# Performance work log

Hardware: AMD Instinct MI355X
Metric: run time of the kernel (lower is better)

## Reference

```python
import jax, jax.numpy as jnp
import numpy as np
from jax import lax

BETA = 0.5          # module default beta
WD_ITERATION = 50   # module default wd_iteration
ERR_TOL = 0.1       # early-exit threshold in IPOT loop
EPS_FILL = 1e-8     # masked_fill value


def setup_inputs() -> dict:
    key = jax.random.key(0)
    k1, k2 = jax.random.split(key)
    bs, N = 128, 512
    # non-negative cost matrix, bs x N x N
    C = jax.random.uniform(k1, (bs, N, N), dtype=jnp.float32)
    # boolean node mask, bs x N; guarantee at least one valid node per graph
    mask = jax.random.uniform(k2, (bs, N)) < 0.8
    mask = mask.at[:, 0].set(True)
    return {"C": C, "bs": bs, "N_s": N, "N_t": N, "mask": mask}


def _ipot_T(C, mask, beta=BETA, iteration=WD_ITERATION):
    m = mask.astype(jnp.float32)                                   # (bs, N)
    mu = (m / jnp.sum(m, axis=1, keepdims=True))[:, :, None]       # (bs, N, 1)
    mv = mu
    T0 = m[:, :, None] * m[:, None, :]                             # bmm(mask, mask^T)
    A = jnp.exp(-C / beta)
    notmask = ~mask[:, :, None]                                    # (bs, N, 1)

    def step(carry, _):
        T, sigma, done = carry
        Q = A * T
        b = jnp.einsum('bnm,bmk->bnk', Q, sigma)                   # Q @ sigma
        b = jnp.where(notmask, EPS_FILL, b)
        delta = mu / b
        a = jnp.einsum('bnm,bnk->bmk', Q, delta)                   # Q^T @ delta
        a = jnp.where(notmask, EPS_FILL, a)
        sigma_new = mv / a
        T_new = delta * Q * jnp.swapaxes(sigma_new, 1, 2)
        err = jnp.max(jnp.sum(jnp.abs(T_new - T), axis=-1))        # global max, as in torch
        # emulate host-side early exit: once converged, freeze state
        T_out = jnp.where(done, T, T_new)
        sigma_out = jnp.where(done, sigma, sigma_new)
        done_out = done | (err < ERR_TOL)
        return (T_out, sigma_out, done_out), None

    (T, _, _), _ = lax.scan(step, (T0, mu, jnp.array(False)), None, length=iteration)
    return T


def reference(C, bs, N_s, N_t, mask):
    T = _ipot_T(C, mask)
    distance = jnp.sum(T * C, axis=(-2, -1))                       # (bs,)
    return (distance, T, C)
```

## Files before the change

kernel.cpp:

```cpp
#include <hip/hip_runtime.h>

#define INVB   2.0f
#define TOL    0.1f
#define EPS    1e-8f
#define NITER  50


__device__ __forceinline__ float wave_sum(float v) {
    for (int o = 32; o > 0; o >>= 1) v += __shfl_down(v, o, 64);
    return v;
}

__global__ __launch_bounds__(1024, 4) void k_ipot_blk(
    const float* __restrict__ C, const void* __restrict__ mraw,
    int bs, int N, float* outD, float* outT, float* outC)
{
    const int bb   = blockIdx.x;
    const int t    = threadIdx.x;
    const int lane = t & 63;
    const int wv   = t >> 6;
    const int nw   = blockDim.x >> 6;
    const float NEG = -__builtin_inff();

    __shared__ __align__(16) float m01[512];
    __shared__ __align__(16) float ld_s[512];
    __shared__ __align__(16) float ldp_s[512];
    __shared__ __align__(16) float ls_s[512];
    __shared__ __align__(16) float lsp_s[512];
    __shared__ __align__(16) float lsig_s[512];
    __shared__ __align__(16) float bv_s[512];
    __shared__ __align__(16) float ap_s[1024];
    __shared__ float red_s[16];
    __shared__ unsigned errbits;
    __shared__ int sF_flag, sB_flag;
    __shared__ float muv_s, lmu_s;

    if (t == 0) { sF_flag = 0; sB_flag = 0; }
    __syncthreads();
    {
        const unsigned* mw = (const unsigned*)mraw;
        const int nwords = (bs * N) >> 2;
        int f = 0, b = 0;
        for (int i = t; i < nwords; i += 1024) {
            unsigned w = mw[i];
            if (w == 0x3f800000u) f = 1;
            else if (w > 1u)      b = 1;
        }
        if (f) atomicOr(&sF_flag, 1);
        if (b) atomicOr(&sB_flag, 1);
    }
    __syncthreads();
    const int mode = sF_flag ? 2 : (sB_flag ? 1 : 0);

    if (t < N) {
        const int idx = bb * N + t;
        bool mv;
        if (mode == 1)      mv = ((const unsigned char*)mraw)[idx] != 0;
        else if (mode == 2) mv = ((const float*)mraw)[idx] != 0.0f;
        else                mv = ((const int*)mraw)[idx] != 0;
        const float z = mv ? 0.f : NEG;
        m01[t]  = mv ? 1.f : 0.f;
        ld_s[t] = z;  ldp_s[t] = z;
        ls_s[t] = z;  lsp_s[t] = z;
    }
    __syncthreads();
    if (wv < (N >> 6)) {
        float v = (t < N) ? m01[t] : 0.f;
        v = wave_sum(v);
        if (lane == 0) red_s[wv] = v;
    }
    __syncthreads();
    if (t == 0) {
        float cnt = 0.f;
        for (int i = 0; i < (N >> 6); ++i) cnt += red_s[i];
        const float muv = 1.0f / cnt;
        muv_s = muv; lmu_s = __logf(muv);
    }
    __syncthreads();
    const float muv = muv_s, lmu = lmu_s;
    if (t < N) lsig_s[t] = (m01[t] != 0.f) ? lmu : NEG;
    __syncthreads();

    const int rpw = N / nw;

    for (int j = 0; j < rpw; ++j) {
        const int n = wv * rpw + j;
        float acc = 0.f;
        if (m01[n] != 0.f) {
            const float* crow = C + ((size_t)bb * N + n) * N;
            for (int m = lane * 4; m < N; m += 256) {
                float4 c4 = *(const float4*)(crow + m);
                float4 m4 = *(const float4*)(&m01[m]);
                acc += m4.x * __expf(lmu - INVB * c4.x);
                acc += m4.y * __expf(lmu - INVB * c4.y);
                acc += m4.z * __expf(lmu - INVB * c4.z);
                acc += m4.w * __expf(lmu - INVB * c4.w);
            }
        }
        acc = wave_sum(acc);
        if (lane == 0) bv_s[n] = acc;
    }
    __syncthreads();

    int kf = NITER;
    for (int it = 0; it < NITER; ++it) {
        const float s1 = (float)it * INVB;
        const float s2 = s1 + INVB;
        const float s3 = s2 + INVB;

        if (t < N) {
            const bool v = m01[t] != 0.f;
            const float mun = v ? muv : 0.f;
            const float bm  = v ? bv_s[t] : EPS;
            const float ldo = ld_s[t];
            ldp_s[t] = ldo;
            ld_s[t]  = ldo + __logf(mun / bm);
        }
        __syncthreads();

        {
            const int h  = t / N;
            const int m  = t - h * N;
            const int n0 = h * (N >> 1);
            const float lsv = ls_s[m];
            const float* cp = C + ((size_t)bb * N + n0) * N + m;
            float acc = 0.f;
            #pragma unroll 8
            for (int i = 0; i < (N >> 1); ++i)
                acc += __expf(ld_s[n0 + i] + lsv - s2 * cp[(size_t)i * N]);
            ap_s[t] = acc;
        }
        __syncthreads();

        if (t < N) {
            const bool v = m01[t] != 0.f;
            const float av  = ap_s[t] + ap_s[t + N];
            const float am  = v ? av : EPS;
            const float mun = v ? muv : 0.f;
            const float lsg = __logf(mun / am);
            const float lso = ls_s[t];
            lsp_s[t]  = lso;
            ls_s[t]   = lso + lsg;
            lsig_s[t] = lsg;
        }
        if (t == 0) errbits = 0u;
        __syncthreads();

        {
            float errmax = 0.f;
            for (int j = 0; j < rpw; ++j) {
                const int n = wv * rpw + j;
                const float ldn = ld_s[n], ldo = ldp_s[n];
                float eacc = 0.f, bacc = 0.f;
                if (m01[n] != 0.f) {
                    const float* crow = C + ((size_t)bb * N + n) * N;
                    for (int m = lane * 4; m < N; m += 256) {
                        float4 c4  = *(const float4*)(crow + m);
                        float4 ln4 = *(const float4*)(&ls_s[m]);
                        float4 lo4 = *(const float4*)(&lsp_s[m]);
                        float4 lg4 = *(const float4*)(&lsig_s[m]);
                        float tn, to;
                        tn = __expf(ldn + ln4.x - s2 * c4.x);
                        to = __expf(ldo + lo4.x - s1 * c4.x);
                        eacc += fabsf(tn - to);
                        bacc += __expf(ldn + ln4.x + lg4.x - s3 * c4.x);
                        tn = __expf(ldn + ln4.y - s2 * c4.y);
                        to = __expf(ldo + lo4.y - s1 * c4.y);
                        eacc += fabsf(tn - to);
                        bacc += __expf(ldn + ln4.y + lg4.y - s3 * c4.y);
                        tn = __expf(ldn + ln4.z - s2 * c4.z);
                        to = __expf(ldo + lo4.z - s1 * c4.z);
                        eacc += fabsf(tn - to);
                        bacc += __expf(ldn + ln4.z + lg4.z - s3 * c4.z);
                        tn = __expf(ldn + ln4.w - s2 * c4.w);
                        to = __expf(ldo + lo4.w - s1 * c4.w);
                        eacc += fabsf(tn - to);
                        bacc += __expf(ldn + ln4.w + lg4.w - s3 * c4.w);
                    }
                }
                bacc = wave_sum(bacc);
                eacc = wave_sum(eacc);
                if (lane == 0) { bv_s[n] = bacc; errmax = fmaxf(errmax, eacc); }
            }
            if (lane == 0) atomicMax(&errbits, __float_as_uint(errmax));
        }
        __syncthreads();

        if (__uint_as_float(errbits) < TOL) { kf = it + 1; break; }
    }

    {
        const float sF = (float)kf * INVB;
        for (int j = 0; j < rpw; ++j) {
            const int n  = wv * rpw + j;
            const int gr = bb * N + n;
            const float ldv = ld_s[n];
            const float* crow = C + (size_t)gr * N;
            float* trow = outT + (size_t)gr * N;
            float* orow = outC + (size_t)gr * N;
            float acc = 0.f;
            for (int m = lane * 4; m < N; m += 256) {
                float4 c4 = *(const float4*)(crow + m);
                float4 l4 = *(const float4*)(&ls_s[m]);
                float4 t4;
                t4.x = __expf(ldv + l4.x - sF * c4.x);
                t4.y = __expf(ldv + l4.y - sF * c4.y);
                t4.z = __expf(ldv + l4.z - sF * c4.z);
                t4.w = __expf(ldv + l4.w - sF * c4.w);
                acc += t4.x * c4.x + t4.y * c4.y + t4.z * c4.z + t4.w * c4.w;
                *(float4*)(trow + m) = t4;
                *(float4*)(orow + m) = c4;
            }
            acc = wave_sum(acc);
            if (lane == 0) bv_s[n] = acc;
        }
    }
    __syncthreads();

    if (t < 256 && t + 256 < N) bv_s[t] += bv_s[t + 256];
    __syncthreads();
    for (int o = 128; o > 0; o >>= 1) {
        if (t < o) bv_s[t] += bv_s[t + o];
        __syncthreads();
    }
    if (t == 0) outD[bb] = bv_s[0];
}

extern "C" void kernel_launch(void* const* d_in, const int* in_sizes, int n_in,
                              void* d_out, int out_size, void* d_ws, size_t ws_size,
                              hipStream_t stream) {
    const float* C    = (const float*)d_in[0];
    const void*  mask = d_in[4];
    const int R  = in_sizes[4];
    const int N  = in_sizes[0] / R;
    const int bs = R / N;

    float* outD = (float*)d_out;
    float* outT = outD + bs;
    float* outC = outT + (size_t)bs * N * N;

    k_ipot_blk<<<bs, 1024, 0, stream>>>(C, mask, bs, N, outD, outT, outC);
}
```

Before: 273.9 us.

## Split each batch across four cooperating blocks with global atomic group barriers

Each batch is now handled by four workgroups, each owning a quarter of the rows, instead of one workgroup per batch. This gives 512 blocks rather than 128 so more of the GPU's compute units are used. The column sums that were a separate strided pass are now fused into the row pass, with partial results exchanged through workspace and spin-wait flags. A separate zeroing kernel also detects the mask dtype. The risks are spin-barrier latency on every iteration, a possible deadlock if the four blocks of a group are not co-resident, and the cost of the extra launch.

```diff
diff --git a/kernel.cpp b/kernel.cpp
--- a/kernel.cpp
+++ b/kernel.cpp
@@ -1,229 +1,306 @@
 #include <hip/hip_runtime.h>
 
-#define INVB   2.0f
-#define TOL    0.1f
-#define EPS    1e-8f
-#define NITER  50
-
-
-__device__ __forceinline__ float wave_sum(float v) {
-    for (int o = 32; o > 0; o >>= 1) v += __shfl_down(v, o, 64);
+#define INVB  2.0f
+#define TOL   0.1f
+#define EPS   1e-8f
+#define NITER 50
+#define NP    4
+
+
+__device__ __forceinline__ float wsum(float v) {
+    #pragma unroll
+    for (int o = 1; o < 64; o <<= 1) v += __shfl_xor(v, o, 64);
     return v;
 }
 
-__global__ __launch_bounds__(1024, 4) void k_ipot_blk(
+__device__ __forceinline__ void group_arrive(unsigned* flagp) {
+    __hip_atomic_fetch_add(flagp, 1u, __ATOMIC_RELEASE, __HIP_MEMORY_SCOPE_AGENT);
+}
+__device__ __forceinline__ void group_wait(unsigned* flagp, unsigned target) {
+    long sp = 0;
+    while (__hip_atomic_load(flagp, __ATOMIC_RELAXED, __HIP_MEMORY_SCOPE_AGENT)
+               < target && sp < (1L << 24)) {
+        __builtin_amdgcn_s_sleep(2); ++sp;
+    }
+    (void)__hip_atomic_load(flagp, __ATOMIC_ACQUIRE, __HIP_MEMORY_SCOPE_AGENT);
+}
+
+__global__ void k_zero(unsigned* ctrl, int ctrlwords, int* mode,
+                       const unsigned* mraw, int nwords) {
+    const int t = threadIdx.x;
+    for (int i = t; i < ctrlwords; i += 1024) ctrl[i] = 0u;
+    __shared__ int sF, sB;
+    if (t == 0) { sF = 0; sB = 0; }
+    __syncthreads();
+    int f = 0, b = 0;
+    for (int i = t; i < nwords; i += 1024) {
+        unsigned w = mraw[i];
+        if (w == 0x3f800000u) f = 1;
+        else if (w > 1u)      b = 1;
+    }
+    if (f) atomicOr(&sF, 1);
+    if (b) atomicOr(&sB, 1);
+    __syncthreads();
+    if (t == 0) *mode = sF ? 2 : (sB ? 1 : 0);
+}
+
+__global__ __launch_bounds__(1024, 8) void k_ipot4(
     const float* __restrict__ C, const void* __restrict__ mraw,
-    int bs, int N, float* outD, float* outT, float* outC)
+    int bs, int N,
+    unsigned* err_u, unsigned* flags, float* dpart, const int* mode_p,
+    float* apart, float* outD, float* outT, float* outC)
 {
-    const int bb   = blockIdx.x;
+    const int g    = blockIdx.x >> 2;
+    const int p    = blockIdx.x & 3;
     const int t    = threadIdx.x;
     const int lane = t & 63;
     const int wv   = t >> 6;
-    const int nw   = blockDim.x >> 6;
+    const int NR   = N >> 2;
+    const int r0   = p * NR;
+    const int rpw  = NR >> 4;
     const float NEG = -__builtin_inff();
-
-    __shared__ __align__(16) float m01[512];
-    __shared__ __align__(16) float ld_s[512];
-    __shared__ __align__(16) float ldp_s[512];
+    unsigned* flagp = &flags[g * 16];
+
     __shared__ __align__(16) float ls_s[512];
     __shared__ __align__(16) float lsp_s[512];
     __shared__ __align__(16) float lsig_s[512];
-    __shared__ __align__(16) float bv_s[512];
-    __shared__ __align__(16) float ap_s[1024];
+    __shared__ __align__(16) float m01[512];
+    __shared__ float ld_own[128], ldp_own[128];
+    __shared__ __align__(16) float ap_ws[16][512];
     __shared__ float red_s[16];
-    __shared__ unsigned errbits;
-    __shared__ int sF_flag, sB_flag;
-    __shared__ float muv_s, lmu_s;
-
-    if (t == 0) { sF_flag = 0; sB_flag = 0; }
-    __syncthreads();
+    __shared__ float muv_s, lmu_s, errg_s;
+    __shared__ unsigned errbits_s;
+
     {
-        const unsigned* mw = (const unsigned*)mraw;
-        const int nwords = (bs * N) >> 2;
-        int f = 0, b = 0;
-        for (int i = t; i < nwords; i += 1024) {
-            unsigned w = mw[i];
-            if (w == 0x3f800000u) f = 1;
-            else if (w > 1u)      b = 1;
-        }
-        if (f) atomicOr(&sF_flag, 1);
-        if (b) atomicOr(&sB_flag, 1);
-    }
-    __syncthreads();
-    const int mode = sF_flag ? 2 : (sB_flag ? 1 : 0);
-
-    if (t < N) {
-        const int idx = bb * N + t;
-        bool mv;
-        if (mode == 1)      mv = ((const unsigned char*)mraw)[idx] != 0;
-        else if (mode == 2) mv = ((const float*)mraw)[idx] != 0.0f;
-        else                mv = ((const int*)mraw)[idx] != 0;
-        const float z = mv ? 0.f : NEG;
-        m01[t]  = mv ? 1.f : 0.f;
-        ld_s[t] = z;  ldp_s[t] = z;
-        ls_s[t] = z;  lsp_s[t] = z;
-    }
-    __syncthreads();
-    if (wv < (N >> 6)) {
-        float v = (t < N) ? m01[t] : 0.f;
-        v = wave_sum(v);
-        if (lane == 0) red_s[wv] = v;
-    }
-    __syncthreads();
-    if (t == 0) {
-        float cnt = 0.f;
-        for (int i = 0; i < (N >> 6); ++i) cnt += red_s[i];
-        const float muv = 1.0f / cnt;
-        muv_s = muv; lmu_s = __logf(muv);
-    }
-    __syncthreads();
+        const int mode = *mode_p;
+        if (t < N) {
+            const int idx = g * N + t;
+            bool mv;
+            if (mode == 1)      mv = ((const unsigned char*)mraw)[idx] != 0;
+            else if (mode == 2) mv = ((const float*)mraw)[idx] != 0.0f;
+            else                mv = ((const int*)mraw)[idx] != 0;
+            m01[t] = mv ? 1.f : 0.f;
+            const float z = mv ? 0.f : NEG;
+            ls_s[t] = z; lsp_s[t] = z;
+        }
+        __syncthreads();
+        if (t < N) {
+            float v = wsum(m01[t]);
+            if (lane == 0) red_s[wv] = v;
+        }
+        __syncthreads();
+        if (t == 0) {
+            float cnt = 0.f;
+            for (int i = 0; i < (N >> 6); ++i) cnt += red_s[i];
+            muv_s = 1.0f / cnt;
+            lmu_s = __logf(muv_s);
+        }
+        __syncthreads();
+        if (t < N) lsig_s[t] = (m01[t] != 0.f) ? lmu_s : NEG;
+        if (t < NR) {
+            const float z = (m01[r0 + t] != 0.f) ? 0.f : NEG;
+            ld_own[t] = z; ldp_own[t] = z;
+        }
+        __syncthreads();
+    }
     const float muv = muv_s, lmu = lmu_s;
-    if (t < N) lsig_s[t] = (m01[t] != 0.f) ? lmu : NEG;
-    __syncthreads();
-
-    const int rpw = N / nw;
-
-    for (int j = 0; j < rpw; ++j) {
-        const int n = wv * rpw + j;
-        float acc = 0.f;
-        if (m01[n] != 0.f) {
-            const float* crow = C + ((size_t)bb * N + n) * N;
-            for (int m = lane * 4; m < N; m += 256) {
-                float4 c4 = *(const float4*)(crow + m);
-                float4 m4 = *(const float4*)(&m01[m]);
-                acc += m4.x * __expf(lmu - INVB * c4.x);
-                acc += m4.y * __expf(lmu - INVB * c4.y);
-                acc += m4.z * __expf(lmu - INVB * c4.z);
-                acc += m4.w * __expf(lmu - INVB * c4.w);
-            }
-        }
-        acc = wave_sum(acc);
-        if (lane == 0) bv_s[n] = acc;
-    }
-    __syncthreads();
+    unsigned rnd = 0;
+
+    {
+        float4 fa[2] = {{0,0,0,0},{0,0,0,0}};
+        for (int j = 0; j < rpw; ++j) {
+            const int lo = wv * rpw + j;
+            const int n  = r0 + lo;
+            const bool valid = m01[n] != 0.f;
+            const float* crow = C + ((size_t)g * N + n) * N;
+            float bacc = 0.f;
+            if (valid) {
+                #pragma unroll
+                for (int mg = 0; mg < 2; ++mg) {
+                    const int mb = mg * 256 + lane * 4;
+                    float4 c4 = *(const float4*)(crow + mb);
+                    float4 m4 = *(const float4*)(&m01[mb]);
+                    bacc += m4.x * __expf(lmu - INVB * c4.x);
+                    bacc += m4.y * __expf(lmu - INVB * c4.y);
+                    bacc += m4.z * __expf(lmu - INVB * c4.z);
+                    bacc += m4.w * __expf(lmu - INVB * c4.w);
+                }
+            }
+            bacc = wsum(bacc);
+            const float ldn1 = valid ? __logf(muv / bacc) : NEG;
+            if (lane == 0) ld_own[lo] = ldn1;
+            if (valid) {
+                #pragma unroll
+                for (int mg = 0; mg < 2; ++mg) {
+                    const int mb = mg * 256 + lane * 4;
+                    float4 c4 = *(const float4*)(crow + mb);
+                    float4 l4 = *(const float4*)(&ls_s[mb]);
+                    fa[mg].x += __expf(ldn1 + l4.x - INVB * c4.x);
+                    fa[mg].y += __expf(ldn1 + l4.y - INVB * c4.y);
+                    fa[mg].z += __expf(ldn1 + l4.z - INVB * c4.z);
+                    fa[mg].w += __expf(ldn1 + l4.w - INVB * c4.w);
+                }
+            }
+        }
+        *(float4*)&ap_ws[wv][lane * 4]       = fa[0];
+        *(float4*)&ap_ws[wv][256 + lane * 4] = fa[1];
+        __syncthreads();
+        if (t < N) {
+            float av = 0.f;
+            #pragma unroll
+            for (int w = 0; w < 16; ++w) av += ap_ws[w][t];
+            apart[((size_t)(g * NP + p)) * N + t] = av;
+        }
+        __syncthreads();
+        ++rnd;
+        if (t == 0) { group_arrive(flagp); group_wait(flagp, NP * rnd); }
+        __syncthreads();
+        if (t < N && m01[t] != 0.f) {
+            float av = 0.f;
+            #pragma unroll
+            for (int q = 0; q < NP; ++q) av += apart[((size_t)(g * NP + q)) * N + t];
+            const float lsg = __logf(muv / av);
+            lsp_s[t] = ls_s[t]; ls_s[t] += lsg; lsig_s[t] = lsg;
+        }
+        __syncthreads();
+    }
 
     int kf = NITER;
     for (int it = 0; it < NITER; ++it) {
         const float s1 = (float)it * INVB;
         const float s2 = s1 + INVB;
         const float s3 = s2 + INVB;
-
+        if (t == 0) errbits_s = 0u;
+        float4 fa[2] = {{0,0,0,0},{0,0,0,0}};
+        float errmax = 0.f;
+        __syncthreads();
+
+        for (int j = 0; j < rpw; ++j) {
+            const int lo = wv * rpw + j;
+            const int n  = r0 + lo;
+            const bool valid = m01[n] != 0.f;
+            const float ldn = ld_own[lo], ldo = ldp_own[lo];
+            const float* crow = C + ((size_t)g * N + n) * N;
+            float eacc = 0.f, bacc = 0.f;
+            if (valid) {
+                #pragma unroll
+                for (int mg = 0; mg < 2; ++mg) {
+                    const int mb = mg * 256 + lane * 4;
+                    float4 c4  = *(const float4*)(crow + mb);
+                    float4 ln4 = *(const float4*)(&ls_s[mb]);
+                    float4 lo4 = *(const float4*)(&lsp_s[mb]);
+                    float4 lg4 = *(const float4*)(&lsig_s[mb]);
+                    float tn, to;
+                    tn = __expf(ldn + ln4.x - s2 * c4.x);
+                    to = __expf(ldo + lo4.x - s1 * c4.x);
+                    eacc += fabsf(tn - to);
+                    bacc += __expf(ldn + ln4.x + lg4.x - s3 * c4.x);
+                    tn = __expf(ldn + ln4.y - s2 * c4.y);
+                    to = __expf(ldo + lo4.y - s1 * c4.y);
+                    eacc += fabsf(tn - to);
+                    bacc += __expf(ldn + ln4.y + lg4.y - s3 * c4.y);
+                    tn = __expf(ldn + ln4.z - s2 * c4.z);
+                    to = __expf(ldo + lo4.z - s1 * c4.z);
+                    eacc += fabsf(tn - to);
+                    bacc += __expf(ldn + ln4.z + lg4.z - s3 * c4.z);
+                    tn = __expf(ldn + ln4.w - s2 * c4.w);
+                    to = __expf(ldo + lo4.w - s1 * c4.w);
+                    eacc += fabsf(tn - to);
+                    bacc += __expf(ldn + ln4.w + lg4.w - s3 * c4.w);
+                }
+            }
+            bacc = wsum(bacc);
+            eacc = wsum(eacc);
+            errmax = fmaxf(errmax, eacc);
+            const float ldn2 = valid ? (ldn + __logf(muv / bacc)) : NEG;
+            if (lane == 0) { ldp_own[lo] = ldn; ld_own[lo] = ldn2; }
+            if (valid) {
+                #pragma unroll
+                for (int mg = 0; mg < 2; ++mg) {
+                    const int mb = mg * 256 + lane * 4;
+                    float4 c4 = *(const float4*)(crow + mb);
+                    float4 l4 = *(const float4*)(&ls_s[mb]);
+                    fa[mg].x += __expf(ldn2 + l4.x - s3 * c4.x);
+                    fa[mg].y += __expf(ldn2 + l4.y - s3 * c4.y);
+                    fa[mg].z += __expf(ldn2 + l4.z - s3 * c4.z);
+                    fa[mg].w += __expf(ldn2 + l4.w - s3 * c4.w);
+                }
+            }
+        }
+        if (lane == 0) atomicMax(&errbits_s, __float_as_uint(errmax));
+        *(float4*)&ap_ws[wv][lane * 4]       = fa[0];
+        *(float4*)&ap_ws[wv][256 + lane * 4] = fa[1];
+        __syncthreads();
         if (t < N) {
-            const bool v = m01[t] != 0.f;
-            const float mun = v ? muv : 0.f;
-            const float bm  = v ? bv_s[t] : EPS;
-            const float ldo = ld_s[t];
-            ldp_s[t] = ldo;
-            ld_s[t]  = ldo + __logf(mun / bm);
-        }
-        __syncthreads();
-
-        {
-            const int h  = t / N;
-            const int m  = t - h * N;
-            const int n0 = h * (N >> 1);
-            const float lsv = ls_s[m];
-            const float* cp = C + ((size_t)bb * N + n0) * N + m;
-            float acc = 0.f;
-            #pragma unroll 8
-            for (int i = 0; i < (N >> 1); ++i)
-                acc += __expf(ld_s[n0 + i] + lsv - s2 * cp[(size_t)i * N]);
-            ap_s[t] = acc;
-        }
-        __syncthreads();
-
-        if (t < N) {
-            const bool v = m01[t] != 0.f;
-            const float av  = ap_s[t] + ap_s[t + N];
-            const float am  = v ? av : EPS;
-            const float mun = v ? muv : 0.f;
-            const float lsg = __logf(mun / am);
-            const float lso = ls_s[t];
-            lsp_s[t]  = lso;
-            ls_s[t]   = lso + lsg;
-            lsig_s[t] = lsg;
-        }
-        if (t == 0) errbits = 0u;
-        __syncthreads();
-
-        {
-            float errmax = 0.f;
-            for (int j = 0; j < rpw; ++j) {
-                const int n = wv * rpw + j;
-                const float ldn = ld_s[n], ldo = ldp_s[n];
-                float eacc = 0.f, bacc = 0.f;
-                if (m01[n] != 0.f) {
-                    const float* crow = C + ((size_t)bb * N + n) * N;
-                    for (int m = lane * 4; m < N; m += 256) {
-                        float4 c4  = *(const float4*)(crow + m);
-                        float4 ln4 = *(const float4*)(&ls_s[m]);
-                        float4 lo4 = *(const float4*)(&lsp_s[m]);
-                        float4 lg4 = *(const float4*)(&lsig_s[m]);
-                        float tn, to;
-                        tn = __expf(ldn + ln4.x - s2 * c4.x);
-                        to = __expf(ldo + lo4.x - s1 * c4.x);
-                        eacc += fabsf(tn - to);
-                        bacc += __expf(ldn + ln4.x + lg4.x - s3 * c4.x);
-                        tn = __expf(ldn + ln4.y - s2 * c4.y);
-                        to = __expf(ldo + lo4.y - s1 * c4.y);
-                        eacc += fabsf(tn - to);
-                        bacc += __expf(ldn + ln4.y + lg4.y - s3 * c4.y);
-                        tn = __expf(ldn + ln4.z - s2 * c4.z);
-                        to = __expf(ldo + lo4.z - s1 * c4.z);
-                        eacc += fabsf(tn - to);
-                        bacc += __expf(ldn + ln4.z + lg4.z - s3 * c4.z);
-                        tn = __expf(ldn + ln4.w - s2 * c4.w);
-                        to = __expf(ldo + lo4.w - s1 * c4.w);
-                        eacc += fabsf(tn - to);
-                        bacc += __expf(ldn + ln4.w + lg4.w - s3 * c4.w);
-                    }
-                }
-                bacc = wave_sum(bacc);
-                eacc = wave_sum(eacc);
-                if (lane == 0) { bv_s[n] = bacc; errmax = fmaxf(errmax, eacc); }
-            }
-            if (lane == 0) atomicMax(&errbits, __float_as_uint(errmax));
-        }
-        __syncthreads();
-
-        if (__uint_as_float(errbits) < TOL) { kf = it + 1; break; }
-    }
-
+            float av = 0.f;
+            #pragma unroll
+            for (int w = 0; w < 16; ++w) av += ap_ws[w][t];
+            apart[((size_t)(g * NP + p)) * N + t] = av;
+        }
+        if (t == 0) atomicMax(&err_u[g * 64 + it], errbits_s);
+        __syncthreads();
+        ++rnd;
+        if (t == 0) {
+            group_arrive(flagp); group_wait(flagp, NP * rnd);
+            errg_s = __uint_as_float(err_u[g * 64 + it]);
+        }
+        __syncthreads();
+        if (errg_s < TOL) { kf = it + 1; break; }
+        if (it == NITER - 1) { kf = NITER; break; }
+        if (t < N && m01[t] != 0.f) {
+            float av = 0.f;
+            #pragma unroll
+            for (int q = 0; q < NP; ++q) av += apart[((size_t)(g * NP + q)) * N + t];
+            const float lsg = __logf(muv / av);
+            lsp_s[t] = ls_s[t]; ls_s[t] += lsg; lsig_s[t] = lsg;
+        }
+        __syncthreads();
+    }
+
+    float dacc = 0.f;
     {
         const float sF = (float)kf * INVB;
         for (int j = 0; j < rpw; ++j) {
-            const int n  = wv * rpw + j;
-            const int gr = bb * N + n;
-            const float ldv = ld_s[n];
+            const int lo = wv * rpw + j;
+            const int gr = g * N + r0 + lo;
+            const float ldv = ldp_own[lo];
             const float* crow = C + (size_t)gr * N;
             float* trow = outT + (size_t)gr * N;
             float* orow = outC + (size_t)gr * N;
-            float acc = 0.f;
-            for (int m = lane * 4; m < N; m += 256) {
-                float4 c4 = *(const float4*)(crow + m);
-                float4 l4 = *(const float4*)(&ls_s[m]);
+            #pragma unroll
+            for (int mg = 0; mg < 2; ++mg) {
+                const int mb = mg * 256 + lane * 4;
+                float4 c4 = *(const float4*)(crow + mb);
+                float4 l4 = *(const float4*)(&ls_s[mb]);
                 float4 t4;
                 t4.x = __expf(ldv + l4.x - sF * c4.x);
                 t4.y = __expf(ldv + l4.y - sF * c4.y);
                 t4.z = __expf(ldv + l4.z - sF * c4.z);
                 t4.w = __expf(ldv + l4.w - sF * c4.w);
-                acc += t4.x * c4.x + t4.y * c4.y + t4.z * c4.z + t4.w * c4.w;
-                *(float4*)(trow + m) = t4;
-                *(float4*)(orow + m) = c4;
-            }
-            acc = wave_sum(acc);
-            if (lane == 0) bv_s[n] = acc;
-        }
-    }
+                dacc += t4.x * c4.x + t4.y * c4.y + t4.z * c4.z + t4.w * c4.w;
+                *(float4*)(trow + mb) = t4;
+                *(float4*)(orow + mb) = c4;
+            }
+        }
+    }
+    dacc = wsum(dacc);
+    if (lane == 0) red_s[wv] = dacc;
     __syncthreads();
-
-    if (t < 256 && t + 256 < N) bv_s[t] += bv_s[t + 256];
-    __syncthreads();
-    for (int o = 128; o > 0; o >>= 1) {
-        if (t < o) bv_s[t] += bv_s[t + o];
-        __syncthreads();
-    }
-    if (t == 0) outD[bb] = bv_s[0];
+    ++rnd;
+    if (t == 0) {
+        float d = 0.f;
+        #pragma unroll
+        for (int w = 0; w < 16; ++w) d += red_s[w];
+        dpart[g * NP + p] = d;
+        group_arrive(flagp);
+        if (p == 0) {
+            group_wait(flagp, NP * rnd);
+            float dt = 0.f;
+            #pragma unroll
+            for (int q = 0; q < NP; ++q) dt += dpart[g * NP + q];
+            outD[g] = dt;
+        }
+    }
 }
 
 extern "C" void kernel_launch(void* const* d_in, const int* in_sizes, int n_in,
@@ -235,9 +312,21 @@
     const int N  = in_sizes[0] / R;
     const int bs = R / N;
 
+    unsigned* wsu   = (unsigned*)d_ws;
+    unsigned* err_u = wsu;
+    unsigned* flags = wsu + (size_t)bs * 64;
+    float*    dpart = (float*)(flags + (size_t)bs * 16);
+    int*      mode  = (int*)(dpart + (size_t)bs * NP);
+    const int ctrlwords = bs * 64 + bs * 16 + bs * NP + 1;
+    float*    apart = (float*)(wsu + ((ctrlwords + 255) & ~255));
+
     float* outD = (float*)d_out;
     float* outT = outD + bs;
     float* outC = outT + (size_t)bs * N * N;
 
-    k_ipot_blk<<<bs, 1024, 0, stream>>>(C, mask, bs, N, outD, outT, outC);
-}
+    k_zero<<<1, 1024, 0, stream>>>(wsu, ctrlwords, mode,
+                                   (const unsigned*)mask, R / 4);
+    k_ipot4<<<bs * NP, 1024, 0, stream>>>(C, mask, bs, N,
+                                          err_u, flags, dpart, mode,
+                                          apart, outD, outT, outC);
+}
```

Result: faster. 236.6 us (median of 2 runs) (-13.6%).
